# Performance work log

Measured on AMD Instinct MI355X. Metric: run time of the kernel, lower is better.

The kernel has to match this reference:

```python
import jax, jax.numpy as jnp
import numpy as np

B, T, HIDDEN = 1, 2048, 2048
N_HEADS, N_KV_HEADS, HEAD_DIM = 32, 8, 64
N_KV_GROUPS = N_HEADS // N_KV_HEADS
MAX_POS = 8192


def _rope_tables(seq_len, head_dim, dtype):
    inv_freq = 1.0 / (10000.0 ** (jnp.arange(0, head_dim, 2, dtype=jnp.float32) / head_dim))
    t = jnp.arange(seq_len, dtype=jnp.float32)
    freqs = jnp.einsum('i,j->ij', t, inv_freq)          # [T, head_dim//2]
    emb = jnp.concatenate([freqs, freqs], axis=-1)      # [T, head_dim]
    cos = jnp.cos(emb)[None, None].astype(dtype)        # [1,1,T,head_dim]
    sin = jnp.sin(emb)[None, None].astype(dtype)
    return cos, sin


def _apply_rotary(x, cos, sin):
    # faithful to original: interleaved rotate-half with cat(freqs,freqs) tables
    x1, x2 = x[..., ::2], x[..., 1::2]
    x_rot = jnp.stack([-x2, x1], axis=-1).reshape(x.shape)
    return x * cos + x_rot * sin


def setup_inputs() -> dict:
    key = jax.random.key(0)
    kx, kq, kk, kv, ko = jax.random.split(key, 5)
    s = 0.02
    return {
        'x':  jax.random.normal(kx, (B, T, HIDDEN), dtype=jnp.float32),
        'Wq': s * jax.random.normal(kq, (N_HEADS * HEAD_DIM, HIDDEN), dtype=jnp.float32),
        'Wk': s * jax.random.normal(kk, (N_KV_HEADS * HEAD_DIM, HIDDEN), dtype=jnp.float32),
        'Wv': s * jax.random.normal(kv, (N_KV_HEADS * HEAD_DIM, HIDDEN), dtype=jnp.float32),
        'Wo': s * jax.random.normal(ko, (HIDDEN, HIDDEN), dtype=jnp.float32),
    }


def reference(x, Wq, Wk, Wv, Wo):
    Bv, Tv, _ = x.shape
    dtype = x.dtype
    # projections (torch Linear: y = x @ W.T), reshape to [B, heads, T, head_dim]
    q = jnp.einsum('bth,oh->bto', x, Wq).reshape(Bv, Tv, N_HEADS, HEAD_DIM).transpose(0, 2, 1, 3)
    k = jnp.einsum('bth,oh->bto', x, Wk).reshape(Bv, Tv, N_KV_HEADS, HEAD_DIM).transpose(0, 2, 1, 3)
    v = jnp.einsum('bth,oh->bto', x, Wv).reshape(Bv, Tv, N_KV_HEADS, HEAD_DIM).transpose(0, 2, 1, 3)
    cos, sin = _rope_tables(Tv, HEAD_DIM, dtype)
    q = _apply_rotary(q, cos, sin)
    k = _apply_rotary(k, cos, sin)
    if N_KV_GROUPS != 1:
        k = jnp.repeat(k, N_KV_GROUPS, axis=1)   # [B, n_heads, T, d]
        v = jnp.repeat(v, N_KV_GROUPS, axis=1)
    scale = 1.0 / jnp.sqrt(jnp.asarray(HEAD_DIM, dtype=dtype))
    scores = jnp.einsum('bhtd,bhsd->bhts', q, k) * scale   # [B,H,T,T]
    causal = jnp.tril(jnp.ones((Tv, Tv), dtype=bool))
    scores = jnp.where(causal[None, None], scores, jnp.asarray(-jnp.inf, dtype=dtype))
    attn = jax.nn.softmax(scores, axis=-1)
    out = jnp.einsum('bhts,bhsd->bhtd', attn, v)
    out = out.transpose(0, 2, 1, 3).reshape(Bv, Tv, HIDDEN)
    return jnp.einsum('bth,oh->bto', out, Wo)
```

## Files before the change

### kernel.cpp

```cpp
#include <hip/hip_runtime.h>
#include <hip/hip_bf16.h>
#include <stdint.h>

#define TT 2048
#define HID 2048
#define NH 32
#define NKV 8
#define HD 64

typedef __attribute__((ext_vector_type(4))) float f32x4;
typedef __attribute__((ext_vector_type(16))) float f32x16;
typedef __attribute__((ext_vector_type(8))) short bf16x8;

__device__ __forceinline__ unsigned short f2bf(float f) {
  unsigned int u = __builtin_bit_cast(unsigned int, f);
  unsigned int r = (u + 0x7FFFu + ((u >> 16) & 1u)) >> 16;
  return (unsigned short)r;
}
__device__ __forceinline__ float bf2f(unsigned short h) {
  unsigned int u = ((unsigned int)h) << 16;
  return __builtin_bit_cast(float, u);
}
__device__ __forceinline__ unsigned int cvtpk(float lo, float hi) {
  unsigned int d;
  asm("v_cvt_pk_bf16_f32 %0, %1, %2" : "=v"(d) : "v"(lo), "v"(hi));
  return d;
}

__device__ __forceinline__ void gld_lds16(const void* g, void* l) {
  __builtin_amdgcn_global_load_lds(
      (const __attribute__((address_space(1))) unsigned int*)g,
      (__attribute__((address_space(3))) unsigned int*)l,
      16, 0, 0);
}

__global__ __launch_bounds__(256)
void k_cvt_all(const float* __restrict__ x, const float* __restrict__ wq,
               const float* __restrict__ wk, const float* __restrict__ wv,
               const float* __restrict__ wo,
               unsigned short* __restrict__ xb, unsigned short* __restrict__ wqb,
               unsigned short* __restrict__ wkb, unsigned short* __restrict__ wvb,
               unsigned short* __restrict__ wob) {
  int i = blockIdx.x * 256 + threadIdx.x;
  const float* src; unsigned short* dst; int off;
  if      (i < 1048576) { src = x;  dst = xb;  off = i; }
  else if (i < 2097152) { src = wq; dst = wqb; off = i - 1048576; }
  else if (i < 2359296) { src = wk; dst = wkb; off = i - 2097152; }
  else if (i < 2621440) { src = wv; dst = wvb; off = i - 2359296; }
  else if (i < 3670016) { src = wo; dst = wob; off = i - 2621440; }
  else return;
  const float4 v = reinterpret_cast<const float4*>(src)[off];
  ushort4 o;
  o.x = f2bf(v.x); o.y = f2bf(v.y); o.z = f2bf(v.z); o.w = f2bf(v.w);
  reinterpret_cast<ushort4*>(dst)[off] = o;
}

__device__ __forceinline__ void stage_tile(const unsigned short* __restrict__ g,
                                           unsigned short* lds, int w, int l, int k0) {
#pragma unroll
  for (int j = 0; j < 2; ++j) {
    const int cbase = w * 128 + j * 64;
    const int c = cbase + l;
    const int row = c >> 2, off = c & 3;
    gld_lds16(g + row * 2048 + k0 + off * 8, lds + cbase * 8);
  }
}

__device__ __forceinline__ void gemm_core(const unsigned short* __restrict__ A,
                                          const unsigned short* __restrict__ B,
                                          unsigned short* As, unsigned short* Bs,
                                          f32x4 (&acc)[4][4], int kiters) {
  const int tid = threadIdx.x;
  const int l = tid & 63, w = tid >> 6;
  const int wm = w >> 1, wn = w & 1;
  const int ll = l & 15, lg = l >> 4;

  stage_tile(A, As, w, l, 0);
  stage_tile(B, Bs, w, l, 0);
  int cur = 0;
  for (int kt = 0; kt < kiters; ++kt) {
    __syncthreads();
    if (kt + 1 < kiters) {
      stage_tile(A, As + (cur ^ 1) * 4096, w, l, (kt + 1) * 32);
      stage_tile(B, Bs + (cur ^ 1) * 4096, w, l, (kt + 1) * 32);
    }
    const unsigned short* a0 = As + cur * 4096;
    const unsigned short* b0 = Bs + cur * 4096;
    bf16x8 af[4], bfr[4];
#pragma unroll
    for (int i = 0; i < 4; ++i) {
      af[i]  = *reinterpret_cast<const bf16x8*>(a0 + (wm * 64 + i * 16 + ll) * 32 + lg * 8);
      bfr[i] = *reinterpret_cast<const bf16x8*>(b0 + (wn * 64 + i * 16 + ll) * 32 + lg * 8);
    }
#pragma unroll
    for (int i = 0; i < 4; ++i)
#pragma unroll
      for (int j = 0; j < 4; ++j)
        acc[i][j] = __builtin_amdgcn_mfma_f32_16x16x32_bf16(af[i], bfr[j], acc[i][j], 0, 0, 0);
    cur ^= 1;
  }
}

__global__ __launch_bounds__(256)
void k_gemm_qkv(const unsigned short* __restrict__ xb,
                const unsigned short* __restrict__ wq,
                const unsigned short* __restrict__ wk,
                const unsigned short* __restrict__ wv,
                unsigned short* __restrict__ Pq,
                unsigned short* __restrict__ Pk,
                unsigned short* __restrict__ Pv) {
  __shared__ __align__(16) unsigned short As[2 * 4096];
  __shared__ __align__(16) unsigned short Bs[2 * 4096];
  const int bid = blockIdx.x;
  const unsigned short *A, *B;
  int m0, n0, seg, ks;
  if (bid < 640) {
    ks = bid & 1;
    int pair = bid >> 1;
    int mt = pair / 20, nt = pair % 20;
    m0 = mt * 128;
    A = xb + (size_t)m0 * 2048 + ks * 1024;
    if (nt < 16) { seg = 0; n0 = nt * 128; B = wq + (size_t)n0 * 2048 + ks * 1024; }
    else         { seg = 1; n0 = (nt - 16) * 128; B = wk + (size_t)n0 * 2048 + ks * 1024; }
  } else {
    int vb = bid - 640;
    ks = vb & 1;
    int pair = vb >> 1;
    int mt = pair / 16, nt = pair % 16;
    seg = 2; m0 = mt * 128; n0 = nt * 128;
    A = wv + (size_t)m0 * 2048 + ks * 1024;
    B = xb + (size_t)n0 * 2048 + ks * 1024;
  }
  f32x4 acc[4][4] = {};
  gemm_core(A, B, As, Bs, acc, 32);

  const int l = threadIdx.x & 63, w = threadIdx.x >> 6;
  const int wm = w >> 1, wn = w & 1;
#pragma unroll
  for (int i = 0; i < 4; ++i)
#pragma unroll
    for (int j = 0; j < 4; ++j)
#pragma unroll
      for (int r = 0; r < 4; ++r) {
        int row = m0 + wm * 64 + i * 16 + ((l >> 4) << 2) + r;
        int col = n0 + wn * 64 + j * 16 + (l & 15);
        unsigned short v = f2bf(acc[i][j][r]);
        if (seg == 0)      Pq[(size_t)ks * 4194304 + (size_t)row * 2048 + col] = v;
        else if (seg == 1) Pk[(size_t)ks * 1048576 + (size_t)row * 512 + col] = v;
        else               Pv[(size_t)ks * 1048576 + (size_t)row * 2048 + col] = v;
      }
}

__global__ __launch_bounds__(256)
void k_gemm_out(const unsigned short* __restrict__ Ob,
                const unsigned short* __restrict__ wo,
                float* __restrict__ out,
                float* __restrict__ p1a, float* __restrict__ p1b) {
  __shared__ __align__(16) unsigned short As[2 * 4096];
  __shared__ __align__(16) unsigned short Bs[2 * 4096];
  const int bid = blockIdx.x;
  const int ks = bid >> 8;
  const int rem = bid & 255;
  const int m0 = (rem >> 4) * 128, n0 = (rem & 15) * 128;
  f32x4 acc[4][4] = {};
  gemm_core(Ob + (size_t)m0 * 2048 + ks * 1024,
            wo + (size_t)n0 * 2048 + ks * 1024, As, Bs, acc, 32);

  const int l = threadIdx.x & 63, w = threadIdx.x >> 6;
  const int wm = w >> 1, wn = w & 1;
#pragma unroll
  for (int i = 0; i < 4; ++i)
#pragma unroll
    for (int j = 0; j < 4; ++j)
#pragma unroll
      for (int r = 0; r < 4; ++r) {
        int row = m0 + wm * 64 + i * 16 + ((l >> 4) << 2) + r;
        int col = n0 + wn * 64 + j * 16 + (l & 15);
        if (ks == 0) {
          out[(size_t)row * HID + col] = acc[i][j][r];
        } else {
          float* p = (row < 1024) ? (p1a + (size_t)row * HID)
                                  : (p1b + (size_t)(row - 1024) * HID);
          p[col] = acc[i][j][r];
        }
      }
}

__global__ __launch_bounds__(256)
void k_reduce_out(float* __restrict__ out,
                  const float* __restrict__ p1a, const float* __restrict__ p1b) {
  const int i = blockIdx.x * 256 + threadIdx.x;
  const int row = i >> 9;
  const float* p1 = (row < 1024) ? p1a : (p1b - (size_t)1024 * HID);
  const float4 a = reinterpret_cast<const float4*>(out)[i];
  const float4 b = reinterpret_cast<const float4*>(p1)[i];
  float4 c;
  c.x = a.x + b.x; c.y = a.y + b.y; c.z = a.z + b.z; c.w = a.w + b.w;
  reinterpret_cast<float4*>(out)[i] = c;
}

__global__ __launch_bounds__(256)
void k_rope_tab(float2* __restrict__ tab) {
  const int i = blockIdx.x * 256 + threadIdx.x;
  const int t = i >> 6, k = i & 63;
  const float cexp = -13.287712379549449f / 32.0f;
  const float fr = exp2f((float)(k & 31) * cexp);
  const float a = (float)t * fr;
  tab[i] = make_float2(__cosf(a), __sinf(a));
}

__global__ __launch_bounds__(256)
void k_rope_apply(const unsigned short* __restrict__ Pk,
                  const unsigned short* __restrict__ Pv,
                  const unsigned short* __restrict__ Pq,
                  const float2* __restrict__ tab,
                  unsigned short* __restrict__ Kb,
                  unsigned short* __restrict__ VT,
                  unsigned short* __restrict__ Qb) {
  int p = blockIdx.x * 256 + threadIdx.x;
  if (p < 524288) {
    const int t = p >> 8;
    const int col2 = (p & 255) * 2;
    const int kh = col2 >> 6, d = col2 & 63;
    const unsigned int u0 = *reinterpret_cast<const unsigned int*>(Pk + (size_t)t * 512 + col2);
    const unsigned int u1 = *reinterpret_cast<const unsigned int*>(Pk + 1048576 + (size_t)t * 512 + col2);
    float x0 = bf2f((unsigned short)(u0 & 0xFFFFu)) + bf2f((unsigned short)(u1 & 0xFFFFu));
    float x1 = bf2f((unsigned short)(u0 >> 16)) + bf2f((unsigned short)(u1 >> 16));
    const float4 cs = *reinterpret_cast<const float4*>(tab + t * 64 + d);
    float o0 = x0 * cs.x - x1 * cs.y;
    float o1 = x1 * cs.z + x0 * cs.w;
    unsigned int pw = (unsigned int)f2bf(o0) | ((unsigned int)f2bf(o1) << 16);
    *reinterpret_cast<unsigned int*>(Kb + ((size_t)kh * 2048 + t) * 64 + d) = pw;
  } else if (p < 1048576) {
    const int i2 = (p - 524288) * 2;
    const unsigned int u0 = *reinterpret_cast<const unsigned int*>(Pv + i2);
    const unsigned int u1 = *reinterpret_cast<const unsigned int*>(Pv + 1048576 + i2);
    float x0 = bf2f((unsigned short)(u0 & 0xFFFFu)) + bf2f((unsigned short)(u1 & 0xFFFFu));
    float x1 = bf2f((unsigned short)(u0 >> 16)) + bf2f((unsigned short)(u1 >> 16));
    unsigned int pw = (unsigned int)f2bf(x0) | ((unsigned int)f2bf(x1) << 16);
    *reinterpret_cast<unsigned int*>(VT + i2) = pw;
  } else {
    const int pq = p - 1048576;
    const int t = pq >> 10;
    const int col2 = (pq & 1023) * 2;
    const int h = col2 >> 6, d = col2 & 63;
    const unsigned int u0 = *reinterpret_cast<const unsigned int*>(Pq + (size_t)t * 2048 + col2);
    const unsigned int u1 = *reinterpret_cast<const unsigned int*>(Pq + 4194304 + (size_t)t * 2048 + col2);
    float x0 = bf2f((unsigned short)(u0 & 0xFFFFu)) + bf2f((unsigned short)(u1 & 0xFFFFu));
    float x1 = bf2f((unsigned short)(u0 >> 16)) + bf2f((unsigned short)(u1 >> 16));
    const float scale = 0.125f * 1.4426950408889634f;
    const float4 cs = *reinterpret_cast<const float4*>(tab + t * 64 + d);
    float o0 = (x0 * cs.x - x1 * cs.y) * scale;
    float o1 = (x1 * cs.z + x0 * cs.w) * scale;
    unsigned int pw = (unsigned int)f2bf(o0) | ((unsigned int)f2bf(o1) << 16);
    *reinterpret_cast<unsigned int*>(Qb + ((size_t)h * 2048 + t) * 64 + d) = pw;
  }
}

__device__ __forceinline__ void attn_stage(const unsigned short* __restrict__ Kg,
                                           const unsigned short* __restrict__ Vg,
                                           unsigned short* Ks, unsigned short* Vs,
                                           int kv0, int w, int l) {
#pragma unroll
  for (int j = 0; j < 4; ++j) {
    const int cb = j * 128 + w * 64;
    const int c = cb + l;
    const int row = c >> 3;
    const int src8 = ((c & 7) ^ (row & 7)) * 8;
    gld_lds16(Kg + (size_t)(kv0 + row) * 64 + src8, Ks + cb * 8);
    gld_lds16(Vg + (size_t)row * TT + kv0 + src8, Vs + cb * 8);
  }
}

__global__ __launch_bounds__(128, 2)
void k_attn(const unsigned short* __restrict__ Qb,
            const unsigned short* __restrict__ Kb,
            const unsigned short* __restrict__ VT,
            unsigned short* __restrict__ Ob) {
  __shared__ __align__(16) unsigned short Ks[2][64 * 64];
  __shared__ __align__(16) unsigned short Vs[2][64 * 64];
  const int b = blockIdx.x;
  const int h = b & 31;
  const int qi = b >> 5;
  const int q0 = qi & 7, kq = qi >> 3;
  const int qt = (kq == 0) ? 2 * q0 : (kq == 1) ? 31 - 2 * q0
               : (kq == 2) ? 2 * q0 + 1 : 30 - 2 * q0;
  const int kh = h >> 2;
  const int tid = threadIdx.x;
  const int l = tid & 63, w = tid >> 6;
  const int q = l & 31, hi = l >> 5;
  const int qrow = qt * 64 + w * 32 + q;

  const unsigned short* Qh = Qb + (size_t)h * TT * 64;
  const unsigned short* Kh = Kb + (size_t)kh * TT * 64;
  const unsigned short* Vh = VT + (size_t)kh * 64 * TT;

  bf16x8 qf[4];
#pragma unroll
  for (int s = 0; s < 4; ++s)
    qf[s] = *reinterpret_cast<const bf16x8*>(Qh + (size_t)qrow * 64 + s * 16 + hi * 8);

  f32x16 ot0, ot1;
#pragma unroll
  for (int r = 0; r < 16; ++r) { ot0[r] = 0.f; ot1[r] = 0.f; }
  float lsum = 0.f;
  const int nkt = qt + 1;

  attn_stage(Kh, Vh, Ks[0], Vs[0], 0, w, l);
  int cur = 0;
  for (int kt = 0; kt < nkt; ++kt) {
    __syncthreads();
    if (kt + 1 < nkt)
      attn_stage(Kh, Vh, Ks[cur ^ 1], Vs[cur ^ 1], (kt + 1) * 64, w, l);

    const char* Kc = reinterpret_cast<const char*>(Ks[cur]);
    const char* Vc = reinterpret_cast<const char*>(Vs[cur]);

    f32x16 s0, s1;
#pragma unroll
    for (int r = 0; r < 16; ++r) { s0[r] = 0.f; s1[r] = 0.f; }
    __builtin_amdgcn_s_setprio(1);
#pragma unroll
    for (int s = 0; s < 4; ++s) {
      const int chunk = 2 * s + hi;
      const bf16x8 kf0 = *reinterpret_cast<const bf16x8*>(
          Kc + q * 128 + ((chunk ^ (q & 7)) * 16));
      const bf16x8 kf1 = *reinterpret_cast<const bf16x8*>(
          Kc + (32 + q) * 128 + ((chunk ^ (q & 7)) * 16));
      s0 = __builtin_amdgcn_mfma_f32_32x32x16_bf16(kf0, qf[s], s0, 0, 0, 0);
      s1 = __builtin_amdgcn_mfma_f32_32x32x16_bf16(kf1, qf[s], s1, 0, 0, 0);
    }
    __builtin_amdgcn_s_setprio(0);
    if (kt == qt) {
#pragma unroll
      for (int r = 0; r < 16; ++r) {
        const int kvr = kt * 64 + (r & 3) + 8 * (r >> 2) + 4 * hi;
        if (kvr > qrow) s0[r] = -3e38f;
        if (kvr + 32 > qrow) s1[r] = -3e38f;
      }
    }
#pragma unroll
    for (int r = 0; r < 16; ++r) {
      s0[r] = __builtin_amdgcn_exp2f(s0[r] - 16.f);
      s1[r] = __builtin_amdgcn_exp2f(s1[r] - 16.f);
    }
    float t16[16];
#pragma unroll
    for (int r = 0; r < 16; ++r) t16[r] = s0[r] + s1[r];
#pragma unroll
    for (int r = 0; r < 8; ++r) t16[r] += t16[r + 8];
#pragma unroll
    for (int r = 0; r < 4; ++r) t16[r] += t16[r + 4];
    lsum += (t16[0] + t16[1]) + (t16[2] + t16[3]);

#pragma unroll
    for (int s = 0; s < 4; ++s) {
      const int base = (s & 1) * 8;
      const f32x16& sg = (s < 2) ? s0 : s1;
      const unsigned int c0 = cvtpk(sg[base + 0], sg[base + 1]);
      const unsigned int c1 = cvtpk(sg[base + 2], sg[base + 3]);
      const unsigned int c2 = cvtpk(sg[base + 4], sg[base + 5]);
      const unsigned int c3 = cvtpk(sg[base + 6], sg[base + 7]);
      const unsigned int slo = hi ? c0 : c2, shi_ = hi ? c1 : c3;
      const unsigned int rlo = (unsigned int)__shfl_xor((int)slo, 32);
      const unsigned int rhi = (unsigned int)__shfl_xor((int)shi_, 32);
      union { unsigned int u[4]; bf16x8 v; } P;
      P.u[0] = hi ? rlo : c0;
      P.u[1] = hi ? rhi : c1;
      P.u[2] = hi ? c2 : rlo;
      P.u[3] = hi ? c3 : rhi;
      const int chunk = 2 * s + hi;
      const bf16x8 vf0 = *reinterpret_cast<const bf16x8*>(
          Vc + q * 128 + ((chunk ^ (q & 7)) * 16));
      const bf16x8 vf1 = *reinterpret_cast<const bf16x8*>(
          Vc + (32 + q) * 128 + ((chunk ^ (q & 7)) * 16));
      __builtin_amdgcn_s_setprio(1);
      ot0 = __builtin_amdgcn_mfma_f32_32x32x16_bf16(vf0, P.v, ot0, 0, 0, 0);
      ot1 = __builtin_amdgcn_mfma_f32_32x32x16_bf16(vf1, P.v, ot1, 0, 0, 0);
      __builtin_amdgcn_s_setprio(0);
    }
    cur ^= 1;
  }

  lsum += __shfl_xor(lsum, 32);
  __syncthreads();
  float* Of = reinterpret_cast<float*>(&Ks[0][0]) + w * (64 * 33);
  const float inv = 1.0f / lsum;
#pragma unroll
  for (int r = 0; r < 16; ++r) {
    const int d = (r & 3) + 8 * (r >> 2) + 4 * hi;
    Of[d * 33 + q] = ot0[r] * inv;
    Of[(d + 32) * 33 + q] = ot1[r] * inv;
  }
  __syncthreads();
#pragma unroll
  for (int i = 0; i < 4; ++i) {
    const int a = 4 * hi + i;
    float v[8];
#pragma unroll
    for (int k2 = 0; k2 < 8; ++k2) v[k2] = Of[(a * 8 + k2) * 33 + q];
    union { unsigned int u[4]; uint4 vec; } O4;
    O4.u[0] = cvtpk(v[0], v[1]);
    O4.u[1] = cvtpk(v[2], v[3]);
    O4.u[2] = cvtpk(v[4], v[5]);
    O4.u[3] = cvtpk(v[6], v[7]);
    *reinterpret_cast<uint4*>(Ob + (size_t)qrow * HID + h * 64 + a * 8) = O4.vec;
  }
}

extern "C" void kernel_launch(void* const* d_in, const int* in_sizes, int n_in,
                              void* d_out, int out_size, void* d_ws, size_t ws_size,
                              hipStream_t stream) {
  const float* x  = (const float*)d_in[0];
  const float* Wq = (const float*)d_in[1];
  const float* Wk = (const float*)d_in[2];
  const float* Wv = (const float*)d_in[3];
  const float* Wo = (const float*)d_in[4];
  float* out = (float*)d_out;
  char* ws = (char*)d_ws;

  unsigned short* xb  = (unsigned short*)(ws);
  unsigned short* wqb = (unsigned short*)(ws + (8u  << 20));
  unsigned short* wkb = (unsigned short*)(ws + (16u << 20));
  unsigned short* wvb = (unsigned short*)(ws + (18u << 20));
  unsigned short* wob = (unsigned short*)(ws + (20u << 20));
  unsigned short* Qb  = (unsigned short*)(ws + (28u << 20));
  unsigned short* Kb  = (unsigned short*)(ws + (36u << 20));
  unsigned short* VT  = (unsigned short*)(ws + (38u << 20));
  unsigned short* Ob  = xb;
  float2* tab = (float2*)(ws + (8u << 20));
  unsigned short* Pq = (unsigned short*)d_out;
  unsigned short* Pk = (unsigned short*)(ws + (28u << 20));
  unsigned short* Pv = (unsigned short*)(ws + (32u << 20));
  float* p1a = (float*)(ws + (8u << 20));
  float* p1b = (float*)(ws + (28u << 20));

  k_cvt_all<<<14336, 256, 0, stream>>>(x, Wq, Wk, Wv, Wo, xb, wqb, wkb, wvb, wob);
  k_gemm_qkv<<<768, 256, 0, stream>>>(xb, wqb, wkb, wvb, Pq, Pk, Pv);
  k_rope_tab<<<512, 256, 0, stream>>>(tab);
  k_rope_apply<<<12288, 256, 0, stream>>>(Pk, Pv, Pq, tab, Kb, VT, Qb);
  k_attn<<<1024, 128, 0, stream>>>(Qb, Kb, VT, Ob);
  k_gemm_out<<<512, 256, 0, stream>>>(Ob, wob, out, p1a, p1b);
  k_reduce_out<<<4096, 256, 0, stream>>>(out, p1a, p1b);
}
```

Baseline: 156.6 us.

## Split output GEMM three ways with bf16 partials; use 32x32x8 MFMA for PV

The output projection now splits K three ways (22/21/21 iterations) across 768 blocks instead of two halves across 512, which should fill more CUs. The two extra partial sums are stored as bf16 and summed in the reduce kernel, which cuts partial-buffer traffic but adds rounding error. In attention, the PV step swaps the 32x32x16 MFMA plus cross-lane shuffles for eight 32x32x8 MFMAs on 4-element fragments. This removes the shuffles and selects but issues twice as many MFMA instructions.

After: 157.1 us. No clear change (+0.3%).

```diff
diff --git a/kernel.cpp b/kernel.cpp
--- a/kernel.cpp
+++ b/kernel.cpp
@@ -11,6 +11,7 @@
 typedef __attribute__((ext_vector_type(4))) float f32x4;
 typedef __attribute__((ext_vector_type(16))) float f32x16;
 typedef __attribute__((ext_vector_type(8))) short bf16x8;
+typedef __attribute__((ext_vector_type(4))) short bf16x4;
 
 __device__ __forceinline__ unsigned short f2bf(float f) {
   unsigned int u = __builtin_bit_cast(unsigned int, f);
@@ -25,6 +26,17 @@
   unsigned int d;
   asm("v_cvt_pk_bf16_f32 %0, %1, %2" : "=v"(d) : "v"(lo), "v"(hi));
   return d;
+}
+
+__device__ __forceinline__ f32x16 mfma_32x8(bf16x4 a, bf16x4 b, f32x16 c) {
+#if __has_builtin(__builtin_amdgcn_mfma_f32_32x32x8bf16_1k)
+  return __builtin_amdgcn_mfma_f32_32x32x8bf16_1k(a, b, c, 0, 0, 0);
+#elif __has_builtin(__builtin_amdgcn_mfma_f32_32x32x8_bf16)
+  return __builtin_amdgcn_mfma_f32_32x32x8_bf16(a, b, c, 0, 0, 0);
+#else
+  asm("v_mfma_f32_32x32x8_bf16 %0, %1, %2, %0" : "+v"(c) : "v"(a), "v"(b));
+  return c;
+#endif
 }
 
 __device__ __forceinline__ void gld_lds16(const void* g, void* l) {
@@ -155,16 +167,19 @@
 void k_gemm_out(const unsigned short* __restrict__ Ob,
                 const unsigned short* __restrict__ wo,
                 float* __restrict__ out,
-                float* __restrict__ p1a, float* __restrict__ p1b) {
+                unsigned short* __restrict__ P1,
+                unsigned short* __restrict__ P2) {
   __shared__ __align__(16) unsigned short As[2 * 4096];
   __shared__ __align__(16) unsigned short Bs[2 * 4096];
   const int bid = blockIdx.x;
   const int ks = bid >> 8;
   const int rem = bid & 255;
   const int m0 = (rem >> 4) * 128, n0 = (rem & 15) * 128;
+  const int k0 = (ks == 0) ? 0 : 704 + (ks - 1) * 672;
+  const int kiters = (ks == 0) ? 22 : 21;
   f32x4 acc[4][4] = {};
-  gemm_core(Ob + (size_t)m0 * 2048 + ks * 1024,
-            wo + (size_t)n0 * 2048 + ks * 1024, As, Bs, acc, 32);
+  gemm_core(Ob + (size_t)m0 * 2048 + k0,
+            wo + (size_t)n0 * 2048 + k0, As, Bs, acc, kiters);
 
   const int l = threadIdx.x & 63, w = threadIdx.x >> 6;
   const int wm = w >> 1, wn = w & 1;
@@ -176,27 +191,25 @@
       for (int r = 0; r < 4; ++r) {
         int row = m0 + wm * 64 + i * 16 + ((l >> 4) << 2) + r;
         int col = n0 + wn * 64 + j * 16 + (l & 15);
-        if (ks == 0) {
-          out[(size_t)row * HID + col] = acc[i][j][r];
-        } else {
-          float* p = (row < 1024) ? (p1a + (size_t)row * HID)
-                                  : (p1b + (size_t)(row - 1024) * HID);
-          p[col] = acc[i][j][r];
-        }
+        if (ks == 0)      out[(size_t)row * HID + col] = acc[i][j][r];
+        else if (ks == 1) P1[(size_t)row * HID + col] = f2bf(acc[i][j][r]);
+        else              P2[(size_t)row * HID + col] = f2bf(acc[i][j][r]);
       }
 }
 
 __global__ __launch_bounds__(256)
 void k_reduce_out(float* __restrict__ out,
-                  const float* __restrict__ p1a, const float* __restrict__ p1b) {
+                  const unsigned short* __restrict__ P1,
+                  const unsigned short* __restrict__ P2) {
   const int i = blockIdx.x * 256 + threadIdx.x;
-  const int row = i >> 9;
-  const float* p1 = (row < 1024) ? p1a : (p1b - (size_t)1024 * HID);
-  const float4 a = reinterpret_cast<const float4*>(out)[i];
-  const float4 b = reinterpret_cast<const float4*>(p1)[i];
-  float4 c;
-  c.x = a.x + b.x; c.y = a.y + b.y; c.z = a.z + b.z; c.w = a.w + b.w;
-  reinterpret_cast<float4*>(out)[i] = c;
+  float4 a = reinterpret_cast<const float4*>(out)[i];
+  const ushort4 b = reinterpret_cast<const ushort4*>(P1)[i];
+  const ushort4 c = reinterpret_cast<const ushort4*>(P2)[i];
+  a.x += bf2f(b.x) + bf2f(c.x);
+  a.y += bf2f(b.y) + bf2f(c.y);
+  a.z += bf2f(b.z) + bf2f(c.z);
+  a.w += bf2f(b.w) + bf2f(c.w);
+  reinterpret_cast<float4*>(out)[i] = a;
 }
 
 __global__ __launch_bounds__(256)
@@ -353,32 +366,21 @@
     for (int r = 0; r < 4; ++r) t16[r] += t16[r + 4];
     lsum += (t16[0] + t16[1]) + (t16[2] + t16[3]);
 
-#pragma unroll
-    for (int s = 0; s < 4; ++s) {
-      const int base = (s & 1) * 8;
-      const f32x16& sg = (s < 2) ? s0 : s1;
-      const unsigned int c0 = cvtpk(sg[base + 0], sg[base + 1]);
-      const unsigned int c1 = cvtpk(sg[base + 2], sg[base + 3]);
-      const unsigned int c2 = cvtpk(sg[base + 4], sg[base + 5]);
-      const unsigned int c3 = cvtpk(sg[base + 6], sg[base + 7]);
-      const unsigned int slo = hi ? c0 : c2, shi_ = hi ? c1 : c3;
-      const unsigned int rlo = (unsigned int)__shfl_xor((int)slo, 32);
-      const unsigned int rhi = (unsigned int)__shfl_xor((int)shi_, 32);
-      union { unsigned int u[4]; bf16x8 v; } P;
-      P.u[0] = hi ? rlo : c0;
-      P.u[1] = hi ? rhi : c1;
-      P.u[2] = hi ? c2 : rlo;
-      P.u[3] = hi ? c3 : rhi;
-      const int chunk = 2 * s + hi;
-      const bf16x8 vf0 = *reinterpret_cast<const bf16x8*>(
-          Vc + q * 128 + ((chunk ^ (q & 7)) * 16));
-      const bf16x8 vf1 = *reinterpret_cast<const bf16x8*>(
-          Vc + (32 + q) * 128 + ((chunk ^ (q & 7)) * 16));
-      __builtin_amdgcn_s_setprio(1);
-      ot0 = __builtin_amdgcn_mfma_f32_32x32x16_bf16(vf0, P.v, ot0, 0, 0, 0);
-      ot1 = __builtin_amdgcn_mfma_f32_32x32x16_bf16(vf1, P.v, ot1, 0, 0, 0);
-      __builtin_amdgcn_s_setprio(0);
-    }
+    __builtin_amdgcn_s_setprio(1);
+#pragma unroll
+    for (int t = 0; t < 8; ++t) {
+      const f32x16& sg = (t < 4) ? s0 : s1;
+      const int tb = (t & 3) * 4;
+      union { unsigned int u[2]; bf16x4 v; } P;
+      P.u[0] = cvtpk(sg[tb + 0], sg[tb + 1]);
+      P.u[1] = cvtpk(sg[tb + 2], sg[tb + 3]);
+      const int bo = ((t ^ (q & 7)) * 16) + 8 * hi;
+      const bf16x4 vf0 = *reinterpret_cast<const bf16x4*>(Vc + q * 128 + bo);
+      const bf16x4 vf1 = *reinterpret_cast<const bf16x4*>(Vc + (32 + q) * 128 + bo);
+      ot0 = mfma_32x8(vf0, P.v, ot0);
+      ot1 = mfma_32x8(vf1, P.v, ot1);
+    }
+    __builtin_amdgcn_s_setprio(0);
     cur ^= 1;
   }
 
@@ -432,14 +434,14 @@
   unsigned short* Pq = (unsigned short*)d_out;
   unsigned short* Pk = (unsigned short*)(ws + (28u << 20));
   unsigned short* Pv = (unsigned short*)(ws + (32u << 20));
-  float* p1a = (float*)(ws + (8u << 20));
-  float* p1b = (float*)(ws + (28u << 20));
+  unsigned short* P1 = (unsigned short*)(ws + (8u  << 20));
+  unsigned short* P2 = (unsigned short*)(ws + (28u << 20));
 
   k_cvt_all<<<14336, 256, 0, stream>>>(x, Wq, Wk, Wv, Wo, xb, wqb, wkb, wvb, wob);
   k_gemm_qkv<<<768, 256, 0, stream>>>(xb, wqb, wkb, wvb, Pq, Pk, Pv);
   k_rope_tab<<<512, 256, 0, stream>>>(tab);
   k_rope_apply<<<12288, 256, 0, stream>>>(Pk, Pv, Pq, tab, Kb, VT, Qb);
   k_attn<<<1024, 128, 0, stream>>>(Qb, Kb, VT, Ob);
-  k_gemm_out<<<512, 256, 0, stream>>>(Ob, wob, out, p1a, p1b);
-  k_reduce_out<<<4096, 256, 0, stream>>>(out, p1a, p1b);
-}
+  k_gemm_out<<<768, 256, 0, stream>>>(Ob, wob, out, P1, P2);
+  k_reduce_out<<<4096, 256, 0, stream>>>(out, P1, P2);
+}
```
